# Kernel optimization log

Measured on AMD Instinct MI355X. Metric: run time of the kernel, lower is better.

The kernel has to match this reference:

```python
import jax, jax.numpy as jnp
import numpy as np

HIDDEN = 1024
BATCH = 16
SEQ = 2048
NEG_INF = -1000000000.0


def setup_inputs() -> dict:
    key = jax.random.key(0)
    k1, k2, k3, k4, k5, k6, k7 = jax.random.split(key, 7)
    scale = 1.0 / np.sqrt(HIDDEN)
    return {
        "query": jax.random.normal(k1, (BATCH, HIDDEN), dtype=jnp.float32),
        "keys": jax.random.normal(k2, (BATCH, SEQ, HIDDEN), dtype=jnp.float32),
        "values": jax.random.normal(k3, (BATCH, SEQ, HIDDEN), dtype=jnp.float32),
        "mask": jax.random.randint(k4, (BATCH, SEQ), 0, 2, dtype=jnp.int32),
        # Learned params (nn.Linear(in, out) weight has shape (out, in); we store transposed for x @ W)
        "W1": jax.random.uniform(k5, (HIDDEN, HIDDEN), dtype=jnp.float32, minval=-scale, maxval=scale),
        "W2": jax.random.uniform(k6, (HIDDEN, HIDDEN), dtype=jnp.float32, minval=-scale, maxval=scale),
        "v": jax.random.uniform(k7, (HIDDEN,), dtype=jnp.float32, minval=-scale, maxval=scale),
    }


def reference(query, keys, values, mask, W1, W2, v):
    # scores = v^T tanh(W1 q + W2 k)
    q_proj = query @ W1                       # (b, h)
    k_proj = jnp.einsum('bsh,hd->bsd', keys, W2)  # (b, s, h)
    scores = jnp.einsum('bsh,h->bs', jnp.tanh(q_proj[:, None, :] + k_proj), v)  # (b, s)
    scores = jnp.where(mask == 0, NEG_INF, scores)
    attention_weights = jax.nn.softmax(scores, axis=1)  # (b, s)
    context = jnp.einsum('bs,bsh->bh', attention_weights, values)  # (b, h)
    return context, attention_weights
```

## Files before the change

### kernel.cpp

```cpp
#include <hip/hip_runtime.h>
#include <hip/hip_bf16.h>
#include <cstdint>
#include <cstddef>

#define HIDDEN 1024
#define BATCH 16
#define SEQ 2048
#define M_TOTAL (BATCH*SEQ)
#define NEG_INF -1000000000.0f

typedef unsigned short u16;
typedef __bf16 bf16x8 __attribute__((ext_vector_type(8)));
typedef unsigned short u16x8 __attribute__((ext_vector_type(8)));
typedef unsigned short u16x4 __attribute__((ext_vector_type(4)));
typedef float f32x4 __attribute__((ext_vector_type(4)));

typedef const __attribute__((address_space(1))) void* gas_ptr;
typedef __attribute__((address_space(3))) void* las_ptr;

__device__ __forceinline__ u16 f2bf(float f) {
    unsigned int x = __float_as_uint(f);
    unsigned int r = (x + 0x7fffu + ((x >> 16) & 1u)) >> 16;
    return (u16)r;
}

__device__ __forceinline__ float fast_tanh(float x) {
    float e = __expf(2.0f * x);
    return 1.0f - 2.0f / (e + 1.0f);
}

__global__ __launch_bounds__(512) void qproj_kernel(
    const float* __restrict__ q, const float* __restrict__ W1,
    float* __restrict__ qp)
{
    const int b  = blockIdx.y;
    const int tl = threadIdx.x & 63;
    const int kc = threadIdx.x >> 6;
    const int n  = blockIdx.x * 64 + tl;
    __shared__ float red[8][64];

    const float* qrow = q + b * HIDDEN;
    float acc = 0.f;
    #pragma unroll 8
    for (int k = kc * 128; k < kc * 128 + 128; ++k)
        acc += qrow[k] * W1[(size_t)k * HIDDEN + n];
    red[kc][tl] = acc;
    __syncthreads();
    if (kc == 0) {
        float s = 0.f;
        #pragma unroll
        for (int i = 0; i < 8; ++i) s += red[i][tl];
        qp[b * HIDDEN + n] = s;
    }
}

__global__ __launch_bounds__(256) void w2t_kernel(
    const float* __restrict__ W2, u16* __restrict__ W2T)
{
    __shared__ float tile[64][65];
    const int n0 = blockIdx.x * 64, k0 = blockIdx.y * 64;
    const int tid = threadIdx.x;
    const int c = tid & 63, rb = tid >> 6;
    #pragma unroll
    for (int i = 0; i < 16; ++i) {
        int r = rb + i * 4;
        tile[r][c] = W2[(size_t)(k0 + r) * HIDDEN + n0 + c];
    }
    __syncthreads();
    #pragma unroll
    for (int i = 0; i < 16; ++i) {
        int r = rb + i * 4;
        W2T[(size_t)(n0 + r) * HIDDEN + k0 + c] = f2bf(tile[c][r]);
    }
}

__global__ __launch_bounds__(256) void conv_kernel(
    const float* __restrict__ in, u16* __restrict__ out)
{
    int i = blockIdx.x * 256 + threadIdx.x;
    float4 f = ((const float4*)in)[i];
    u16x4 p;
    p[0] = f2bf(f.x); p[1] = f2bf(f.y); p[2] = f2bf(f.z); p[3] = f2bf(f.w);
    ((u16x4*)out)[i] = p;
}

#define NT3 16

#define WAIT4 asm volatile("s_waitcnt vmcnt(4)" ::: "memory")
#define WAIT2 asm volatile("s_waitcnt vmcnt(2)" ::: "memory")
#define WAIT0 asm volatile("s_waitcnt vmcnt(0)" ::: "memory")
#define NOWAIT do {} while (0)

#define SBAR() do { __builtin_amdgcn_s_barrier(); \
                    asm volatile("" ::: "memory"); } while (0)

#define STAGE_HALF(SRC, ROW0, KT, LBASE)                                    \
    do {                                                                    \
        _Pragma("unroll")                                                   \
        for (int r_ = 0; r_ < 2; ++r_) {                                    \
            int idx_ = r_ * 512 + tid;                                      \
            int row_ = idx_ >> 3, c_ = idx_ & 7;                            \
            const u16* s_ = (SRC) + (size_t)((ROW0) + row_) * HIDDEN        \
                            + (KT) + ((c_ ^ (row_ & 7)) << 3);              \
            las_ptr d_ = (las_ptr)((char*)(LBASE)                           \
                            + (size_t)(r_ * 512 + (wave << 6)) * 16);       \
            __builtin_amdgcn_global_load_lds((gas_ptr)s_, d_, 16, 0, 0);    \
        }                                                                   \
    } while (0)

#define LDFRAG(LBASE, ROWL, CH) __builtin_bit_cast(bf16x8,                  \
    *(const u16x8*)((LBASE) + (ROWL) * 64 + ((((CH) ^ ((ROWL) & 7))) << 3)))

#define PHASE(MS, NS, LOADA, STAGECODE, WAITCODE)                           \
    do {                                                                    \
        if (LOADA) {                                                        \
            _Pragma("unroll")                                               \
            for (int i_ = 0; i_ < 4; ++i_) {                                \
                int rowa_ = (MS) * 128 + wr * 64 + i_ * 16 + c16;           \
                af[i_][0] = LDFRAG(Acur, rowa_, quad);                      \
                af[i_][1] = LDFRAG(Acur, rowa_, 4 + quad);                  \
            }                                                               \
        }                                                                   \
        _Pragma("unroll")                                                   \
        for (int jj_ = 0; jj_ < 2; ++jj_) {                                 \
            int rowb_ = (NS) * 128 + wc * 32 + jj_ * 16 + c16;              \
            bfr[jj_][0] = LDFRAG(Bcur, rowb_, quad);                        \
            bfr[jj_][1] = LDFRAG(Bcur, rowb_, 4 + quad);                    \
        }                                                                   \
        STAGECODE;                                                          \
        WAITCODE;                                                           \
        SBAR();                                                             \
        __builtin_amdgcn_s_setprio(1);                                      \
        _Pragma("unroll")                                                   \
        for (int i_ = 0; i_ < 4; ++i_)                                      \
            _Pragma("unroll")                                               \
            for (int jj_ = 0; jj_ < 2; ++jj_) {                             \
                acc[MS][i_][NS][jj_] =                                      \
                    __builtin_amdgcn_mfma_f32_16x16x32_bf16(                \
                        af[i_][0], bfr[jj_][0], acc[MS][i_][NS][jj_],0,0,0);\
                acc[MS][i_][NS][jj_] =                                      \
                    __builtin_amdgcn_mfma_f32_16x16x32_bf16(                \
                        af[i_][1], bfr[jj_][1], acc[MS][i_][NS][jj_],0,0,0);\
            }                                                               \
        __builtin_amdgcn_s_setprio(0);                                      \
        SBAR();                                                             \
    } while (0)

__global__ __launch_bounds__(512) void scores_v3_kernel(
    const u16*   __restrict__ keysb,
    const u16*   __restrict__ W2T,
    const float* __restrict__ qp,
    const float* __restrict__ v,
    float*       __restrict__ part)
{
    __shared__ __align__(16) u16 lds[65536];

    const int tid = threadIdx.x;
    const int lid = blockIdx.x + (blockIdx.y << 2);
    const int xcd = lid & 7;
    const int j8  = lid >> 3;
    const int nt  = j8 & 3;
    const int mt  = (xcd << 4) + (j8 >> 2);
    const int m0  = mt << 8;
    const int n0  = nt << 8;

    const int wave = tid >> 6, lane = tid & 63;
    const int wr = wave >> 2;
    const int wc = wave & 3;
    const int quad = lane >> 4, c16 = lane & 15;

    const u16* Akeys = keysb + (size_t)m0 * HIDDEN;
    const u16* Bw2t  = W2T   + (size_t)n0 * HIDDEN;

    f32x4 acc[2][4][2][2];
    #pragma unroll
    for (int a = 0; a < 2; ++a)
        #pragma unroll
        for (int i = 0; i < 4; ++i)
            #pragma unroll
            for (int c = 0; c < 2; ++c)
                #pragma unroll
                for (int d = 0; d < 2; ++d)
                    acc[a][i][c][d] = f32x4{0.f, 0.f, 0.f, 0.f};

    bf16x8 af[4][2], bfr[2][2];

    STAGE_HALF(Akeys, 0,   0, (char*)lds + 0);
    STAGE_HALF(Bw2t,  0,   0, (char*)lds + 65536);
    STAGE_HALF(Bw2t,  128, 0, (char*)lds + 65536 + 16384);
    STAGE_HALF(Akeys, 128, 0, (char*)lds + 16384);
    WAIT0;
    SBAR();

    for (int T = 0; T < NT3 - 1; ++T) {
        const int p = T & 1;
        const u16* Acur = (const u16*)((const char*)lds + p * 32768);
        const u16* Bcur = (const u16*)((const char*)lds + 65536 + p * 32768);
        char* Anext = (char*)lds + (p ^ 1) * 32768;
        char* Bnext = (char*)lds + 65536 + (p ^ 1) * 32768;
        const int ktn = (T + 1) * 64;

        PHASE(0, 0, true,  STAGE_HALF(Akeys, 0,   ktn, Anext),         WAIT4);
        PHASE(0, 1, false, STAGE_HALF(Bw2t,  0,   ktn, Bnext),         WAIT4);
        PHASE(1, 0, true,  STAGE_HALF(Bw2t,  128, ktn, Bnext + 16384), WAIT4);
        PHASE(1, 1, false, STAGE_HALF(Akeys, 128, ktn, Anext + 16384), WAIT4);
    }
    {
        const u16* Acur = (const u16*)((const char*)lds + 32768);
        const u16* Bcur = (const u16*)((const char*)lds + 65536 + 32768);
        PHASE(0, 0, true,  NOWAIT, WAIT2);
        PHASE(0, 1, false, NOWAIT, WAIT0);
        PHASE(1, 0, true,  NOWAIT, NOWAIT);
        PHASE(1, 1, false, NOWAIT, NOWAIT);
    }

    const int b = m0 >> 11;
    float qv[2][2], vv[2][2];
    #pragma unroll
    for (int ns = 0; ns < 2; ++ns)
        #pragma unroll
        for (int jj = 0; jj < 2; ++jj) {
            int n = n0 + ns * 128 + wc * 32 + jj * 16 + c16;
            qv[ns][jj] = qp[b * HIDDEN + n];
            vv[ns][jj] = v[n];
        }
    const int slot = (nt << 2) + wc;
    #pragma unroll
    for (int ms = 0; ms < 2; ++ms)
        #pragma unroll
        for (int i = 0; i < 4; ++i)
            #pragma unroll
            for (int r = 0; r < 4; ++r) {
                float s = 0.f;
                #pragma unroll
                for (int ns = 0; ns < 2; ++ns)
                    #pragma unroll
                    for (int jj = 0; jj < 2; ++jj)
                        s += fast_tanh(acc[ms][i][ns][jj][r] + qv[ns][jj])
                             * vv[ns][jj];
                s += __shfl_xor(s, 1);
                s += __shfl_xor(s, 2);
                s += __shfl_xor(s, 4);
                s += __shfl_xor(s, 8);
                if (c16 == 0) {
                    int m = m0 + ms * 128 + wr * 64 + i * 16 + quad * 4 + r;
                    part[(size_t)slot * M_TOTAL + m] = s;
                }
            }
}

#define BM 128
#define BN 128
#define BK 64
#define LDA 72

__global__ __launch_bounds__(256) void scores_v1_kernel(
    const float* __restrict__ keys,
    const u16*   __restrict__ W2T,
    const float* __restrict__ qp,
    const float* __restrict__ v,
    float*       __restrict__ part)
{
    __shared__ __align__(16) u16 Alds[BM][LDA];
    __shared__ __align__(16) u16 Blds[BN][LDA];

    const int tid  = threadIdx.x;
    const int nt   = blockIdx.x;
    const int n0   = nt * BN;
    const int m0   = blockIdx.y * BM;
    const int wave = tid >> 6, lane = tid & 63;
    const int wr = wave >> 1, wc = wave & 1;
    const int quad = lane >> 4, c16 = lane & 15;

    f32x4 acc[4][4];
    #pragma unroll
    for (int i = 0; i < 4; ++i)
        #pragma unroll
        for (int jj = 0; jj < 4; ++jj)
            acc[i][jj] = f32x4{0.f, 0.f, 0.f, 0.f};

    for (int kt = 0; kt < HIDDEN; kt += BK) {
        __syncthreads();
        const float* gA = keys + (size_t)m0 * HIDDEN + kt;
        #pragma unroll
        for (int i = 0; i < 8; ++i) {
            int idx = tid + i * 256;
            int r = idx >> 4, c4 = idx & 15;
            float4 f = *(const float4*)(gA + (size_t)r * HIDDEN + c4 * 4);
            u16x4 pk;
            pk[0] = f2bf(f.x); pk[1] = f2bf(f.y);
            pk[2] = f2bf(f.z); pk[3] = f2bf(f.w);
            *(u16x4*)&Alds[r][c4 * 4] = pk;
        }
        #pragma unroll
        for (int i = 0; i < 4; ++i) {
            int idx = tid + i * 256;
            int r = idx >> 3, c8 = idx & 7;
            uint4 raw = ((const uint4*)(W2T + (size_t)(n0 + r) * HIDDEN + kt))[c8];
            *(uint4*)&Blds[r][c8 * 8] = raw;
        }
        __syncthreads();

        #pragma unroll
        for (int ks = 0; ks < BK; ks += 32) {
            bf16x8 af[4], bfr[4];
            #pragma unroll
            for (int i = 0; i < 4; ++i)
                af[i] = __builtin_bit_cast(bf16x8,
                    *(const u16x8*)&Alds[wr * 64 + i * 16 + c16][ks + quad * 8]);
            #pragma unroll
            for (int jj = 0; jj < 4; ++jj)
                bfr[jj] = __builtin_bit_cast(bf16x8,
                    *(const u16x8*)&Blds[wc * 64 + jj * 16 + c16][ks + quad * 8]);
            #pragma unroll
            for (int i = 0; i < 4; ++i)
                #pragma unroll
                for (int jj = 0; jj < 4; ++jj)
                    acc[i][jj] = __builtin_amdgcn_mfma_f32_16x16x32_bf16(
                        af[i], bfr[jj], acc[i][jj], 0, 0, 0);
        }
    }

    const int b = m0 >> 11;
    float qv[4], vv[4];
    #pragma unroll
    for (int jj = 0; jj < 4; ++jj) {
        int n = n0 + wc * 64 + jj * 16 + c16;
        qv[jj] = qp[b * HIDDEN + n];
        vv[jj] = v[n];
    }
    const int slot = nt * 2 + wc;
    #pragma unroll
    for (int i = 0; i < 4; ++i) {
        #pragma unroll
        for (int r = 0; r < 4; ++r) {
            float s = 0.f;
            #pragma unroll
            for (int jj = 0; jj < 4; ++jj)
                s += fast_tanh(acc[i][jj][r] + qv[jj]) * vv[jj];
            s += __shfl_xor(s, 1);
            s += __shfl_xor(s, 2);
            s += __shfl_xor(s, 4);
            s += __shfl_xor(s, 8);
            if (c16 == 0) {
                int m = m0 + wr * 64 + i * 16 + quad * 4 + r;
                part[(size_t)slot * M_TOTAL + m] = s;
            }
        }
    }
}

__global__ __launch_bounds__(1024) void softmax_kernel(
    const float* __restrict__ part, const int* __restrict__ mask,
    float* __restrict__ attn)
{
    const int b = blockIdx.x, tid = threadIdx.x;
    const int wave = tid >> 6, lane = tid & 63;
    __shared__ float red[16];
    float sc[2];
    float mx = -1e30f;
    #pragma unroll
    for (int j = 0; j < 2; ++j) {
        int s = tid + j * 1024;
        float a = 0.f;
        #pragma unroll
        for (int p = 0; p < 16; ++p)
            a += part[(size_t)p * M_TOTAL + b * SEQ + s];
        if (mask[b * SEQ + s] == 0) a = NEG_INF;
        sc[j] = a;
        mx = fmaxf(mx, a);
    }
    #pragma unroll
    for (int o = 32; o > 0; o >>= 1) mx = fmaxf(mx, __shfl_xor(mx, o));
    if (lane == 0) red[wave] = mx;
    __syncthreads();
    #pragma unroll
    for (int w = 0; w < 16; ++w) mx = fmaxf(mx, red[w]);
    float sum = 0.f;
    #pragma unroll
    for (int j = 0; j < 2; ++j) { sc[j] = __expf(sc[j] - mx); sum += sc[j]; }
    #pragma unroll
    for (int o = 32; o > 0; o >>= 1) sum += __shfl_xor(sum, o);
    __syncthreads();
    if (lane == 0) red[wave] = sum;
    __syncthreads();
    sum = 0.f;
    #pragma unroll
    for (int w = 0; w < 16; ++w) sum += red[w];
    float inv = 1.0f / sum;
    #pragma unroll
    for (int j = 0; j < 2; ++j)
        attn[b * SEQ + tid + j * 1024] = sc[j] * inv;
}

__global__ __launch_bounds__(256) void ctx_part_kernel(
    const float* __restrict__ values, const float* __restrict__ attn,
    float* __restrict__ ctxp)
{
    const int b = blockIdx.x, sch = blockIdx.y, tid = threadIdx.x;
    __shared__ float w[32];
    if (tid < 32) w[tid] = attn[b * SEQ + sch * 32 + tid];
    __syncthreads();
    float4 acc = {0.f, 0.f, 0.f, 0.f};
    const float4* V = (const float4*)(values
        + (size_t)b * SEQ * HIDDEN + (size_t)sch * 32 * HIDDEN);
    #pragma unroll 4
    for (int s = 0; s < 32; ++s) {
        float wv = w[s];
        if (wv != 0.0f) {
            float4 x = V[(size_t)s * (HIDDEN / 4) + tid];
            acc.x += wv * x.x; acc.y += wv * x.y;
            acc.z += wv * x.z; acc.w += wv * x.w;
        }
    }
    ((float4*)(ctxp + (size_t)(b * 64 + sch) * HIDDEN))[tid] = acc;
}

__global__ __launch_bounds__(256) void ctx_reduce_kernel(
    const float* __restrict__ ctxp, float* __restrict__ ctx)
{
    const int b = blockIdx.x, tid = threadIdx.x;
    float4 acc = {0.f, 0.f, 0.f, 0.f};
    const float4* P = (const float4*)(ctxp + (size_t)b * 64 * HIDDEN);
    #pragma unroll 8
    for (int s = 0; s < 64; ++s) {
        float4 x = P[(size_t)s * (HIDDEN / 4) + tid];
        acc.x += x.x; acc.y += x.y; acc.z += x.z; acc.w += x.w;
    }
    ((float4*)(ctx + (size_t)b * HIDDEN))[tid] = acc;
}

extern "C" void kernel_launch(void* const* d_in, const int* in_sizes, int n_in,
                              void* d_out, int out_size, void* d_ws, size_t ws_size,
                              hipStream_t stream)
{
    const float* query  = (const float*)d_in[0];
    const float* keys   = (const float*)d_in[1];
    const float* values = (const float*)d_in[2];
    const int*   mask   = (const int*)d_in[3];
    const float* W1     = (const float*)d_in[4];
    const float* W2     = (const float*)d_in[5];
    const float* v      = (const float*)d_in[6];
    float* out = (float*)d_out;

    char* ws = (char*)d_ws;
    float* qp     = (float*)ws;
    u16*   w2t    = (u16*)(ws + (64 << 10));
    float* part   = (float*)(ws + (64 << 10) + (2 << 20));
    float* ctxp   = (float*)(ws + (64 << 10) + (4 << 20));
    u16*   keysb  = (u16*)(ws + (64 << 10) + (8 << 20));
    const size_t WS_BIG = (64 << 10) + (8 << 20) + ((size_t)64 << 20);

    float* attn_out = out + BATCH * HIDDEN;

    qproj_kernel<<<dim3(16, 16), 512, 0, stream>>>(query, W1, qp);
    w2t_kernel  <<<dim3(16, 16), 256, 0, stream>>>(W2, w2t);

    if (ws_size >= WS_BIG) {
        conv_kernel<<<32768, 256, 0, stream>>>(keys, keysb);
        scores_v3_kernel<<<dim3(4, 128), 512, 0, stream>>>(
            keysb, w2t, qp, v, part);
        softmax_kernel<<<16, 1024, 0, stream>>>(part, mask, attn_out);
        ctx_part_kernel<<<dim3(16, 64), 256, 0, stream>>>(
            values, attn_out, ctxp);
        ctx_reduce_kernel<<<16, 256, 0, stream>>>(ctxp, out);
    } else {
        scores_v1_kernel<<<dim3(8, 256), 256, 0, stream>>>(
            keys, w2t, qp, v, part);
        softmax_kernel<<<16, 1024, 0, stream>>>(part, mask, attn_out);
        if (ws_size >= (64 << 10) + (8 << 20)) {
            ctx_part_kernel<<<dim3(16, 64), 256, 0, stream>>>(
                values, attn_out, ctxp);
            ctx_reduce_kernel<<<16, 256, 0, stream>>>(ctxp, out);
        } else {
            hipMemsetAsync(d_out, 0, BATCH * HIDDEN * sizeof(float), stream);
            ctx_part_kernel<<<dim3(16, 64), 256, 0, stream>>>(
                values, attn_out, (float*)d_ws);
            ctx_reduce_kernel<<<16, 256, 0, stream>>>((float*)d_ws, out);
        }
    }
}
```

Baseline: 376.6 us.

## Fuse fp32-to-bf16 key conversion into the scores GEMM staging

Result: slower. 401.8 us (+6.7%).

```diff
diff --git a/kernel.cpp b/kernel.cpp
--- a/kernel.cpp
+++ b/kernel.cpp
@@ -22,6 +22,12 @@
     unsigned int x = __float_as_uint(f);
     unsigned int r = (x + 0x7fffu + ((x >> 16) & 1u)) >> 16;
     return (u16)r;
+}
+
+__device__ __forceinline__ unsigned cvt_pk_bf16(float lo, float hi) {
+    unsigned r;
+    asm("v_cvt_pk_bf16_f32 %0, %1, %2" : "=v"(r) : "v"(lo), "v"(hi));
+    return r;
 }
 
 __device__ __forceinline__ float fast_tanh(float x) {
@@ -74,35 +80,45 @@
     }
 }
 
-__global__ __launch_bounds__(256) void conv_kernel(
-    const float* __restrict__ in, u16* __restrict__ out)
-{
-    int i = blockIdx.x * 256 + threadIdx.x;
-    float4 f = ((const float4*)in)[i];
-    u16x4 p;
-    p[0] = f2bf(f.x); p[1] = f2bf(f.y); p[2] = f2bf(f.z); p[3] = f2bf(f.w);
-    ((u16x4*)out)[i] = p;
-}
-
-#define NT3 16
-
-#define WAIT4 asm volatile("s_waitcnt vmcnt(4)" ::: "memory")
-#define WAIT2 asm volatile("s_waitcnt vmcnt(2)" ::: "memory")
-#define WAIT0 asm volatile("s_waitcnt vmcnt(0)" ::: "memory")
-#define NOWAIT do {} while (0)
+#define NT4 16
+
+#define WAITV(N) asm volatile("s_waitcnt vmcnt(" #N ")" ::: "memory")
+#define WAITLGKM0 asm volatile("s_waitcnt lgkmcnt(0)" ::: "memory")
 
 #define SBAR() do { __builtin_amdgcn_s_barrier(); \
                     asm volatile("" ::: "memory"); } while (0)
 
-#define STAGE_HALF(SRC, ROW0, KT, LBASE)                                    \
+#define A_LOAD(DST, HALF, KT)                                               \
+    do {                                                                    \
+        _Pragma("unroll")                                                   \
+        for (int h_ = 0; h_ < 4; ++h_)                                      \
+            DST[h_] = *(const float4*)(keys                                 \
+                + (size_t)(m0 + (HALF) * 128 + arow + h_ * 32) * HIDDEN     \
+                + (KT) + ac * 4);                                           \
+    } while (0)
+
+#define A_WRITE(SRC, LOFF)                                                  \
+    do {                                                                    \
+        _Pragma("unroll")                                                   \
+        for (int h_ = 0; h_ < 4; ++h_) {                                    \
+            int row_ = arow + h_ * 32;                                      \
+            unsigned lo_ = cvt_pk_bf16(SRC[h_].x, SRC[h_].y);               \
+            unsigned hi_ = cvt_pk_bf16(SRC[h_].z, SRC[h_].w);               \
+            int byte_ = row_ * 128 + (((ac >> 1) ^ (row_ & 7)) << 4)        \
+                        + ((ac & 1) << 3);                                  \
+            *(uint2*)((char*)lds + (LOFF) + byte_) = make_uint2(lo_, hi_);  \
+        }                                                                   \
+    } while (0)
+
+#define STAGE_B(ROW0, KT, LOFF)                                             \
     do {                                                                    \
         _Pragma("unroll")                                                   \
         for (int r_ = 0; r_ < 2; ++r_) {                                    \
             int idx_ = r_ * 512 + tid;                                      \
             int row_ = idx_ >> 3, c_ = idx_ & 7;                            \
-            const u16* s_ = (SRC) + (size_t)((ROW0) + row_) * HIDDEN        \
+            const u16* s_ = W2T + (size_t)(n0 + (ROW0) + row_) * HIDDEN     \
                             + (KT) + ((c_ ^ (row_ & 7)) << 3);              \
-            las_ptr d_ = (las_ptr)((char*)(LBASE)                           \
+            las_ptr d_ = (las_ptr)((char*)lds + (LOFF)                      \
                             + (size_t)(r_ * 512 + (wave << 6)) * 16);       \
             __builtin_amdgcn_global_load_lds((gas_ptr)s_, d_, 16, 0, 0);    \
         }                                                                   \
@@ -111,7 +127,7 @@
 #define LDFRAG(LBASE, ROWL, CH) __builtin_bit_cast(bf16x8,                  \
     *(const u16x8*)((LBASE) + (ROWL) * 64 + ((((CH) ^ ((ROWL) & 7))) << 3)))
 
-#define PHASE(MS, NS, LOADA, STAGECODE, WAITCODE)                           \
+#define PHASE(MS, NS, LOADA, ...)                                           \
     do {                                                                    \
         if (LOADA) {                                                        \
             _Pragma("unroll")                                               \
@@ -127,8 +143,7 @@
             bfr[jj_][0] = LDFRAG(Bcur, rowb_, quad);                        \
             bfr[jj_][1] = LDFRAG(Bcur, rowb_, 4 + quad);                    \
         }                                                                   \
-        STAGECODE;                                                          \
-        WAITCODE;                                                           \
+        __VA_ARGS__;                                                        \
         SBAR();                                                             \
         __builtin_amdgcn_s_setprio(1);                                      \
         _Pragma("unroll")                                                   \
@@ -146,8 +161,8 @@
         SBAR();                                                             \
     } while (0)
 
-__global__ __launch_bounds__(512) void scores_v3_kernel(
-    const u16*   __restrict__ keysb,
+__global__ __launch_bounds__(512) void scores_v4_kernel(
+    const float* __restrict__ keys,
     const u16*   __restrict__ W2T,
     const float* __restrict__ qp,
     const float* __restrict__ v,
@@ -169,8 +184,8 @@
     const int wc = wave & 3;
     const int quad = lane >> 4, c16 = lane & 15;
 
-    const u16* Akeys = keysb + (size_t)m0 * HIDDEN;
-    const u16* Bw2t  = W2T   + (size_t)n0 * HIDDEN;
+    const int arow = tid >> 4;
+    const int ac   = tid & 15;
 
     f32x4 acc[2][4][2][2];
     #pragma unroll
@@ -184,34 +199,45 @@
                     acc[a][i][c][d] = f32x4{0.f, 0.f, 0.f, 0.f};
 
     bf16x8 af[4][2], bfr[2][2];
-
-    STAGE_HALF(Akeys, 0,   0, (char*)lds + 0);
-    STAGE_HALF(Bw2t,  0,   0, (char*)lds + 65536);
-    STAGE_HALF(Bw2t,  128, 0, (char*)lds + 65536 + 16384);
-    STAGE_HALF(Akeys, 128, 0, (char*)lds + 16384);
-    WAIT0;
+    float4 a0[4], a1[4];
+
+    A_LOAD(a0, 0, 0);
+    STAGE_B(0, 0, 65536);
+    A_LOAD(a1, 1, 0);
+    STAGE_B(128, 0, 65536 + 16384);
+    WAITV(8);
+    A_WRITE(a0, 0);
+    WAITV(2);
+    A_WRITE(a1, 16384);
+    WAITV(0);
+    WAITLGKM0;
     SBAR();
 
-    for (int T = 0; T < NT3 - 1; ++T) {
+    for (int T = 0; T < NT4 - 1; ++T) {
         const int p = T & 1;
         const u16* Acur = (const u16*)((const char*)lds + p * 32768);
         const u16* Bcur = (const u16*)((const char*)lds + 65536 + p * 32768);
-        char* Anext = (char*)lds + (p ^ 1) * 32768;
-        char* Bnext = (char*)lds + 65536 + (p ^ 1) * 32768;
+        const int aoff = (p ^ 1) * 32768;
+        const int boff = 65536 + (p ^ 1) * 32768;
         const int ktn = (T + 1) * 64;
 
-        PHASE(0, 0, true,  STAGE_HALF(Akeys, 0,   ktn, Anext),         WAIT4);
-        PHASE(0, 1, false, STAGE_HALF(Bw2t,  0,   ktn, Bnext),         WAIT4);
-        PHASE(1, 0, true,  STAGE_HALF(Bw2t,  128, ktn, Bnext + 16384), WAIT4);
-        PHASE(1, 1, false, STAGE_HALF(Akeys, 128, ktn, Anext + 16384), WAIT4);
+        PHASE(0, 0, true,
+              A_LOAD(a0, 0, ktn); STAGE_B(0, ktn, boff); WAITV(6));
+        PHASE(0, 1, false,
+              WAITV(2); A_WRITE(a0, aoff);
+              A_LOAD(a1, 1, ktn); STAGE_B(128, ktn, boff + 16384));
+        PHASE(1, 0, true,
+              WAITV(2); A_WRITE(a1, aoff + 16384));
+        PHASE(1, 1, false,
+              WAITLGKM0);
     }
     {
         const u16* Acur = (const u16*)((const char*)lds + 32768);
         const u16* Bcur = (const u16*)((const char*)lds + 65536 + 32768);
-        PHASE(0, 0, true,  NOWAIT, WAIT2);
-        PHASE(0, 1, false, NOWAIT, WAIT0);
-        PHASE(1, 0, true,  NOWAIT, NOWAIT);
-        PHASE(1, 1, false, NOWAIT, NOWAIT);
+        PHASE(0, 0, true,  WAITV(0));
+        PHASE(0, 1, false, );
+        PHASE(1, 0, true,  );
+        PHASE(1, 1, false, );
     }
 
     const int b = m0 >> 11;
@@ -448,18 +474,16 @@
     u16*   w2t    = (u16*)(ws + (64 << 10));
     float* part   = (float*)(ws + (64 << 10) + (2 << 20));
     float* ctxp   = (float*)(ws + (64 << 10) + (4 << 20));
-    u16*   keysb  = (u16*)(ws + (64 << 10) + (8 << 20));
-    const size_t WS_BIG = (64 << 10) + (8 << 20) + ((size_t)64 << 20);
+    const size_t WS_V4 = (64 << 10) + (8 << 20);
 
     float* attn_out = out + BATCH * HIDDEN;
 
     qproj_kernel<<<dim3(16, 16), 512, 0, stream>>>(query, W1, qp);
     w2t_kernel  <<<dim3(16, 16), 256, 0, stream>>>(W2, w2t);
 
-    if (ws_size >= WS_BIG) {
-        conv_kernel<<<32768, 256, 0, stream>>>(keys, keysb);
-        scores_v3_kernel<<<dim3(4, 128), 512, 0, stream>>>(
-            keysb, w2t, qp, v, part);
+    if (ws_size >= WS_V4) {
+        scores_v4_kernel<<<dim3(4, 128), 512, 0, stream>>>(
+            keys, w2t, qp, v, part);
         softmax_kernel<<<16, 1024, 0, stream>>>(part, mask, attn_out);
         ctx_part_kernel<<<dim3(16, 64), 256, 0, stream>>>(
             values, attn_out, ctxp);
```
